# Kernel optimization log

Hardware: AMD Instinct MI355X
Metric: run time of the kernel (lower is better)

Reference implementation:

```python
import jax, jax.numpy as jnp
import numpy as np

NU, NB, NI, D, L = 30000, 10000, 60000, 64, 2
E_UB, E_UI, E_BI = 400000, 800000, 800000


def _graphs(rng, na, nb, ne):
    # random bipartite graph [na, nb] with ne edges; returns Laplacian-normalized
    # symmetric propagation edge list (size 2*ne over na+nb nodes) and the
    # row-normalized aggregation edge values (original MultiCBR preprocessing).
    r = rng.integers(0, na, ne).astype(np.int32)
    c = rng.integers(0, nb, ne).astype(np.int32)
    da = np.bincount(r, minlength=na).astype(np.float32)  # row degrees
    db = np.bincount(c, minlength=nb).astype(np.float32)  # col degrees
    lap = 1.0 / ((np.sqrt(da[r]) + 1e-8) * (np.sqrt(db[c]) + 1e-8))
    prop_rows = np.concatenate([r, c + na]).astype(np.int32)
    prop_cols = np.concatenate([c + na, r]).astype(np.int32)
    prop_vals = np.concatenate([lap, lap]).astype(np.float32)
    agg_vals = (1.0 / (da[r] + 1e-8)).astype(np.float32)  # diag(1/rowsum) @ G
    return prop_rows, prop_cols, prop_vals, r, c, agg_vals


def setup_inputs() -> dict:
    rng = np.random.default_rng(0)
    key = jax.random.key(0)
    ku, kb, ki = jax.random.split(key, 3)
    ub = _graphs(rng, NU, NB, E_UB)
    ui = _graphs(rng, NU, NI, E_UI)
    bi = _graphs(rng, NB, NI, E_BI)
    xav = lambda n: float(np.sqrt(2.0 / (n + D)))  # xavier_normal std
    return {
        "users_feature": jax.random.normal(ku, (NU, D), jnp.float32) * xav(NU),
        "bundles_feature": jax.random.normal(kb, (NB, D), jnp.float32) * xav(NB),
        "items_feature": jax.random.normal(ki, (NI, D), jnp.float32) * xav(NI),
        "ub_rows": jnp.asarray(ub[0]), "ub_cols": jnp.asarray(ub[1]), "ub_vals": jnp.asarray(ub[2]),
        "ui_rows": jnp.asarray(ui[0]), "ui_cols": jnp.asarray(ui[1]), "ui_vals": jnp.asarray(ui[2]),
        "bi_rows": jnp.asarray(bi[0]), "bi_cols": jnp.asarray(bi[1]), "bi_vals": jnp.asarray(bi[2]),
        "bi_agg_rows": jnp.asarray(bi[3]), "bi_agg_cols": jnp.asarray(bi[4]), "bi_agg_vals": jnp.asarray(bi[5]),
        "ui_agg_rows": jnp.asarray(ui[3]), "ui_agg_cols": jnp.asarray(ui[4]), "ui_agg_vals": jnp.asarray(ui[5]),
        "ub_layer_coefs": jnp.full((L + 1,), 1.0 / (L + 1), jnp.float32),
        "ui_layer_coefs": jnp.full((L + 1,), 1.0 / (L + 1), jnp.float32),
        "bi_layer_coefs": jnp.full((L + 1,), 1.0 / (L + 1), jnp.float32),
        "modal_coefs": jnp.asarray([0.4, 0.3, 0.3], jnp.float32),
    }


def _spmm(rows, cols, vals, feat, n):
    # sparse [n, n_src] @ feat : gather + weighted segment-sum
    return jax.ops.segment_sum(vals[:, None] * feat[cols], rows, num_segments=n)


def _l2norm(x):
    # torch F.normalize(p=2, dim=1)
    return x / jnp.maximum(jnp.linalg.norm(x, axis=1, keepdims=True), 1e-12)


def _propagate(rows, cols, vals, a, b, coefs):
    feat = jnp.concatenate([a, b], axis=0)
    n = feat.shape[0]
    acc = coefs[0] * feat  # layer-0 (un-normalized, as in original)
    for i in range(L):
        feat = _spmm(rows, cols, vals, feat, n)
        acc = acc + coefs[i + 1] * _l2norm(feat)
    return acc[: a.shape[0]], acc[a.shape[0]:]


def reference(users_feature, bundles_feature, items_feature,
              ub_rows, ub_cols, ub_vals,
              ui_rows, ui_cols, ui_vals,
              bi_rows, bi_cols, bi_vals,
              bi_agg_rows, bi_agg_cols, bi_agg_vals,
              ui_agg_rows, ui_agg_cols, ui_agg_vals,
              ub_layer_coefs, ui_layer_coefs, bi_layer_coefs, modal_coefs):
    # test=True path of get_multi_modal_representations
    ub_u, ub_b = _propagate(ub_rows, ub_cols, ub_vals, users_feature, bundles_feature, ub_layer_coefs)
    ui_u, ui_i = _propagate(ui_rows, ui_cols, ui_vals, users_feature, items_feature, ui_layer_coefs)
    bi_b, bi_i = _propagate(bi_rows, bi_cols, bi_vals, bundles_feature, items_feature, bi_layer_coefs)
    ui_b = _spmm(bi_agg_rows, bi_agg_cols, bi_agg_vals, ui_i, NB)  # BI_agg @ UI_items
    bi_u = _spmm(ui_agg_rows, ui_agg_cols, ui_agg_vals, bi_i, NU)  # UI_agg @ BI_items
    users_rep = modal_coefs[0] * ub_u + modal_coefs[1] * ui_u + modal_coefs[2] * bi_u
    bundles_rep = modal_coefs[0] * ub_b + modal_coefs[1] * ui_b + modal_coefs[2] * bi_b
    return users_rep, bundles_rep
```

## Files before the change

kernel.cpp:

```cpp
#include <hip/hip_runtime.h>

#define D 64
#define WIN 2048

__device__ __forceinline__ float blo(unsigned u) { return __uint_as_float(u << 16); }
__device__ __forceinline__ float bhi(unsigned u) { return __uint_as_float(u & 0xffff0000u); }
__device__ __forceinline__ unsigned rne(float f) {
    unsigned u = __float_as_uint(f);
    return (u + 0x7fffu + ((u >> 16) & 1u)) >> 16;
}
__device__ __forceinline__ unsigned packbf(float a, float b) {
    unsigned ub = __float_as_uint(b);
    return rne(a) | ((ub + 0x7fffu + ((ub >> 16) & 1u)) & 0xffff0000u);
}
__device__ __forceinline__ void add4(float4* p, float a, float b, float c, float d) {
    float4 o = *p; o.x += a; o.y += b; o.z += c; o.w += d; *p = o;
}

__global__ void to_bf16_kernel(const float* __restrict__ u, const float* __restrict__ b,
                               const float* __restrict__ it,
                               unsigned* __restrict__ SU, unsigned* __restrict__ SB,
                               unsigned* __restrict__ SI, int nU2, int nB2, int nI2) {
    int i = blockIdx.x * 256 + threadIdx.x;
    if (i < nU2) {
        float2 f = ((const float2*)u)[i];
        SU[i] = packbf(f.x, f.y);
    } else if (i < nU2 + nB2) {
        int j = i - nU2;
        float2 f = ((const float2*)b)[j];
        SB[j] = packbf(f.x, f.y);
    } else if (i < nU2 + nB2 + nI2) {
        int j = i - nU2 - nB2;
        float2 f = ((const float2*)it)[j];
        SI[j] = packbf(f.x, f.y);
    }
}

__global__ void hist_kernel(const int* __restrict__ r0, const int* __restrict__ r1,
                            const int* __restrict__ r2,
                            int ne0, int ne1, int ne2, int n0, int n1, int n2,
                            int* __restrict__ histG) {
    __shared__ int h[512];
    int t = threadIdx.x;
    int g = blockIdx.x >> 8, blk = blockIdx.x & 255;
    const int* rows = (g == 0) ? r0 : (g == 1) ? r1 : r2;
    int ne = (g == 0) ? ne0 : (g == 1) ? ne1 : ne2;
    unsigned n = (unsigned)((g == 0) ? n0 : (g == 1) ? n1 : n2);
    h[t] = 0; h[t + 256] = 0;
    __syncthreads();
    int C = (ne + 255) >> 8;
    int e0 = blk * C, e1 = min(ne, e0 + C);
    for (int e = e0 + t; e < e1; e += 256) {
        unsigned b = ((unsigned)rows[e] << 9) / n;
        atomicAdd(&h[b], 1);
    }
    __syncthreads();
    histG[(((g << 9) | t) << 8) | blk] = h[t];
    histG[(((g << 9) | (t + 256)) << 8) | blk] = h[t + 256];
}

__global__ void scan1_kernel(const int* __restrict__ deg, int* __restrict__ rs,
                             int* __restrict__ bsum, int n) {
    __shared__ int tmp[256];
    int t = threadIdx.x;
    int g = blockIdx.x * 256 + t;
    int v = (g < n) ? deg[g] : 0;
    tmp[t] = v;
    __syncthreads();
    for (int off = 1; off < 256; off <<= 1) {
        int x = (t >= off) ? tmp[t - off] : 0;
        __syncthreads();
        tmp[t] += x;
        __syncthreads();
    }
    if (g < n) rs[g] = tmp[t] - v;
    if (t == 255) bsum[blockIdx.x] = tmp[255];
}

__global__ void scan2_kernel(int* __restrict__ bsum, int B) {
    __shared__ int tmp[2048];
    int t = threadIdx.x;
    int v0 = (t < B) ? bsum[t] : 0;
    int v1 = (t + 1024 < B) ? bsum[t + 1024] : 0;
    tmp[t] = v0; tmp[t + 1024] = v1;
    __syncthreads();
    for (int off = 1; off < 2048; off <<= 1) {
        int a0 = (t >= off) ? tmp[t - off] : 0;
        int a1 = ((t + 1024) >= off) ? tmp[t + 1024 - off] : 0;
        __syncthreads();
        tmp[t] += a0; tmp[t + 1024] += a1;
        __syncthreads();
    }
    if (t < B) bsum[t] = tmp[t] - v0;
    if (t + 1024 < B) bsum[t + 1024] = tmp[t + 1024] - v1;
}

__global__ void scan3_kernel(int* __restrict__ rs, const int* __restrict__ bsum, int n) {
    int g = blockIdx.x * blockDim.x + threadIdx.x;
    if (g < n) rs[g] += bsum[g >> 8];
}

__global__ void bucket_scatter_kernel(const int* __restrict__ r0, const int* __restrict__ c0,
                                      const int* __restrict__ r1, const int* __restrict__ c1,
                                      const int* __restrict__ r2, const int* __restrict__ c2,
                                      int ne0, int ne1, int ne2, int n0, int n1, int n2,
                                      const int* __restrict__ hofs, unsigned* __restrict__ ebuf) {
    __shared__ int cur[512];
    int t = threadIdx.x;
    int g = blockIdx.x >> 8, blk = blockIdx.x & 255;
    const int* rows = (g == 0) ? r0 : (g == 1) ? r1 : r2;
    const int* cols = (g == 0) ? c0 : (g == 1) ? c1 : c2;
    int ne = (g == 0) ? ne0 : (g == 1) ? ne1 : ne2;
    int n  = (g == 0) ? n0  : (g == 1) ? n1  : n2;
    cur[t] = hofs[(((g << 9) | t) << 8) | blk];
    cur[t + 256] = hofs[(((g << 9) | (t + 256)) << 8) | blk];
    __syncthreads();
    int C = (ne + 255) >> 8;
    int e0 = blk * C, e1 = min(ne, e0 + C);
    for (int e = e0 + t; e < e1; e += 256) {
        int r = rows[e];
        unsigned b = ((unsigned)r << 9) / (unsigned)n;
        int rb0 = ((int)b * n + 511) >> 9;
        int pos = atomicAdd(&cur[b], 1);
        ebuf[pos] = ((unsigned)(r - rb0) << 23) | (unsigned)cols[e];
    }
}

__global__ void sort_bucket_kernel(const unsigned* __restrict__ ebuf, const int* __restrict__ hofs,
                                   int* __restrict__ rs0, int* __restrict__ rs1, int* __restrict__ rs2,
                                   float* __restrict__ isd0, float* __restrict__ isd1,
                                   float* __restrict__ isd2, int* __restrict__ ccol,
                                   int ne0, int ne1, int ne2, int n0, int n1, int n2) {
    __shared__ int cnt[256];
    __shared__ int pfx[256];
    int t = threadIdx.x;
    int g = blockIdx.x >> 9, b = blockIdx.x & 511;
    int ne = (g == 0) ? ne0 : (g == 1) ? ne1 : ne2;
    int n  = (g == 0) ? n0  : (g == 1) ? n1  : n2;
    int O  = (g == 0) ? 0   : (g == 1) ? ne0 : ne0 + ne1;
    int*   rs  = (g == 0) ? rs0  : (g == 1) ? rs1  : rs2;
    float* isd = (g == 0) ? isd0 : (g == 1) ? isd1 : isd2;
    int rb0 = (b * n + 511) >> 9;
    int rb1 = ((b + 1) * n + 511) >> 9;
    int R = rb1 - rb0;
    cnt[t] = 0;
    __syncthreads();
    int base = hofs[((g << 9) | b) << 8];
    int end  = (b == 511) ? (O + ne) : hofs[((g << 9) | (b + 1)) << 8];
    for (int e = base + t; e < end; e += 256)
        atomicAdd(&cnt[ebuf[e] >> 23], 1);
    __syncthreads();
    pfx[t] = cnt[t];
    __syncthreads();
    for (int off = 1; off < 256; off <<= 1) {
        int v = (t >= off) ? pfx[t - off] : 0;
        __syncthreads();
        pfx[t] += v;
        __syncthreads();
    }
    int c0 = cnt[t], ex = pfx[t] - c0;
    if (t < R) {
        rs[rb0 + t] = base + ex - O;
        isd[rb0 + t] = 1.0f / (sqrtf((float)c0) + 1e-8f);
    }
    __syncthreads();
    cnt[t] = base + ex;
    __syncthreads();
    for (int e = base + t; e < end; e += 256) {
        unsigned p = ebuf[e];
        int pos = atomicAdd(&cnt[p >> 23], 1);
        ccol[pos] = (int)(p & 0x7fffffu);
    }
    if (b == 511 && t == 0) rs[n] = ne;
}

__device__ __forceinline__ int row_deg(int list, int r, const int* rs_ui, const int* rs_bi,
                                       const int* rs_ub, int n_ui, int NU) {
    const int* rs; int rr;
    if (list == 0) { if (r < n_ui) { rs = rs_ui; rr = r; } else { rs = rs_bi; rr = r - n_ui; } }
    else if (list == 1) { rs = rs_ub; rr = r; }
    else { if (r < NU) { rs = rs_ui; rr = r; } else { rs = rs_bi; rr = r - NU; } }
    return rs[rr + 1] - rs[rr];
}

__global__ void winsort_kernel(const int* __restrict__ rs_ui, const int* __restrict__ rs_bi,
                               const int* __restrict__ rs_ub,
                               int n_ui, int NU, int n0, int n1, int n2,
                               int w0, int w1,
                               int* __restrict__ perm0, int* __restrict__ perm1,
                               int* __restrict__ perm2) {
    __shared__ int hist[256];
    __shared__ int pfx[256];
    int t = threadIdx.x;
    int blk = blockIdx.x, list, wbase, n; int* perm;
    if (blk < w0)           { list = 0; wbase = blk * WIN;             n = n0; perm = perm0; }
    else if (blk < w0 + w1) { list = 1; wbase = (blk - w0) * WIN;      n = n1; perm = perm1; }
    else                    { list = 2; wbase = (blk - w0 - w1) * WIN; n = n2; perm = perm2; }
    hist[t] = 0;
    __syncthreads();
    int lim = min(n - wbase, WIN);
    int bins[8], ranks[8];
#pragma unroll
    for (int i = 0; i < 8; ++i) {
        int rr = i * 256 + t;
        if (rr < lim) {
            int d = row_deg(list, wbase + rr, rs_ui, rs_bi, rs_ub, n_ui, NU);
            int b = 255 - min(d, 255);
            bins[i] = b;
            ranks[i] = atomicAdd(&hist[b], 1);
        } else bins[i] = -1;
    }
    __syncthreads();
    int h = hist[t];
    pfx[t] = h;
    __syncthreads();
    for (int off = 1; off < 256; off <<= 1) {
        int x = (t >= off) ? pfx[t - off] : 0;
        __syncthreads();
        pfx[t] += x;
        __syncthreads();
    }
    hist[t] = pfx[t] - h;
    __syncthreads();
#pragma unroll
    for (int i = 0; i < 8; ++i)
        if (bins[i] >= 0) perm[wbase + hist[bins[i]] + ranks[i]] = wbase + i * 256 + t;
}

struct GA {
    const int* rs; const int* ccol; const float* isd;
    const unsigned* srcA; const unsigned* srcB; int na;
    const float* inA; const float* inB;
    unsigned* feat_out; float* dst0; void* dst1;
    const float* coefs; const float* modalp; int mi; int n;
};

template <bool FIRST, bool A0, bool A1, bool BF16D1>
__global__ void spmm_norm_kernel(GA A, GA B, const int* __restrict__ perm, int ntot) {
    int lane = threadIdx.x & 63;
    int row = (blockIdx.x * (blockDim.x >> 6) + (threadIdx.x >> 6)) * 8 + (lane >> 3);
    if (row >= ntot) return;
    row = perm[row];
    GA G; int r;
    if (row < A.n) { G = A; r = row; }
    else           { G = B; r = row - A.n; if (r >= G.n) return; }
    int q = lane & 7;
    int s = G.rs[r], e = G.rs[r + 1];
    float isr = G.isd[r];
    const unsigned* src; int coff;
    if (FIRST && r < G.na) { src = G.srcB; coff = G.na; }
    else                   { src = G.srcA; coff = 0; }
    src += (q << 2);
    const int* cc = G.ccol;
    const float* isdp = G.isd;
    float a[8];
#pragma unroll
    for (int j = 0; j < 8; ++j) a[j] = 0.f;
    int k = s;
    for (; k + 3 < e; k += 4) {
        int c0 = cc[k], c1 = cc[k + 1], c2 = cc[k + 2], c3 = cc[k + 3];
        uint4 f0 = *(const uint4*)(src + (size_t)(c0 - coff) * 32);
        uint4 f1 = *(const uint4*)(src + (size_t)(c1 - coff) * 32);
        uint4 f2 = *(const uint4*)(src + (size_t)(c2 - coff) * 32);
        uint4 f3 = *(const uint4*)(src + (size_t)(c3 - coff) * 32);
        if (FIRST) {
            float v0 = isdp[c0], v1 = isdp[c1], v2 = isdp[c2], v3 = isdp[c3];
            a[0] = fmaf(v0, blo(f0.x), a[0]); a[1] = fmaf(v0, bhi(f0.x), a[1]);
            a[2] = fmaf(v0, blo(f0.y), a[2]); a[3] = fmaf(v0, bhi(f0.y), a[3]);
            a[4] = fmaf(v0, blo(f0.z), a[4]); a[5] = fmaf(v0, bhi(f0.z), a[5]);
            a[6] = fmaf(v0, blo(f0.w), a[6]); a[7] = fmaf(v0, bhi(f0.w), a[7]);
            a[0] = fmaf(v1, blo(f1.x), a[0]); a[1] = fmaf(v1, bhi(f1.x), a[1]);
            a[2] = fmaf(v1, blo(f1.y), a[2]); a[3] = fmaf(v1, bhi(f1.y), a[3]);
            a[4] = fmaf(v1, blo(f1.z), a[4]); a[5] = fmaf(v1, bhi(f1.z), a[5]);
            a[6] = fmaf(v1, blo(f1.w), a[6]); a[7] = fmaf(v1, bhi(f1.w), a[7]);
            a[0] = fmaf(v2, blo(f2.x), a[0]); a[1] = fmaf(v2, bhi(f2.x), a[1]);
            a[2] = fmaf(v2, blo(f2.y), a[2]); a[3] = fmaf(v2, bhi(f2.y), a[3]);
            a[4] = fmaf(v2, blo(f2.z), a[4]); a[5] = fmaf(v2, bhi(f2.z), a[5]);
            a[6] = fmaf(v2, blo(f2.w), a[6]); a[7] = fmaf(v2, bhi(f2.w), a[7]);
            a[0] = fmaf(v3, blo(f3.x), a[0]); a[1] = fmaf(v3, bhi(f3.x), a[1]);
            a[2] = fmaf(v3, blo(f3.y), a[2]); a[3] = fmaf(v3, bhi(f3.y), a[3]);
            a[4] = fmaf(v3, blo(f3.z), a[4]); a[5] = fmaf(v3, bhi(f3.z), a[5]);
            a[6] = fmaf(v3, blo(f3.w), a[6]); a[7] = fmaf(v3, bhi(f3.w), a[7]);
        } else {
            a[0] += blo(f0.x) + blo(f1.x); a[1] += bhi(f0.x) + bhi(f1.x);
            a[2] += blo(f0.y) + blo(f1.y); a[3] += bhi(f0.y) + bhi(f1.y);
            a[4] += blo(f0.z) + blo(f1.z); a[5] += bhi(f0.z) + bhi(f1.z);
            a[6] += blo(f0.w) + blo(f1.w); a[7] += bhi(f0.w) + bhi(f1.w);
            a[0] += blo(f2.x) + blo(f3.x); a[1] += bhi(f2.x) + bhi(f3.x);
            a[2] += blo(f2.y) + blo(f3.y); a[3] += bhi(f2.y) + bhi(f3.y);
            a[4] += blo(f2.z) + blo(f3.z); a[5] += bhi(f2.z) + bhi(f3.z);
            a[6] += blo(f2.w) + blo(f3.w); a[7] += bhi(f2.w) + bhi(f3.w);
        }
    }
    for (; k + 1 < e; k += 2) {
        int c0 = cc[k], c1 = cc[k + 1];
        uint4 f0 = *(const uint4*)(src + (size_t)(c0 - coff) * 32);
        uint4 f1 = *(const uint4*)(src + (size_t)(c1 - coff) * 32);
        if (FIRST) {
            float v0 = isdp[c0], v1 = isdp[c1];
            a[0] = fmaf(v0, blo(f0.x), a[0]); a[1] = fmaf(v0, bhi(f0.x), a[1]);
            a[2] = fmaf(v0, blo(f0.y), a[2]); a[3] = fmaf(v0, bhi(f0.y), a[3]);
            a[4] = fmaf(v0, blo(f0.z), a[4]); a[5] = fmaf(v0, bhi(f0.z), a[5]);
            a[6] = fmaf(v0, blo(f0.w), a[6]); a[7] = fmaf(v0, bhi(f0.w), a[7]);
            a[0] = fmaf(v1, blo(f1.x), a[0]); a[1] = fmaf(v1, bhi(f1.x), a[1]);
            a[2] = fmaf(v1, blo(f1.y), a[2]); a[3] = fmaf(v1, bhi(f1.y), a[3]);
            a[4] = fmaf(v1, blo(f1.z), a[4]); a[5] = fmaf(v1, bhi(f1.z), a[5]);
            a[6] = fmaf(v1, blo(f1.w), a[6]); a[7] = fmaf(v1, bhi(f1.w), a[7]);
        } else {
            a[0] += blo(f0.x) + blo(f1.x); a[1] += bhi(f0.x) + bhi(f1.x);
            a[2] += blo(f0.y) + blo(f1.y); a[3] += bhi(f0.y) + bhi(f1.y);
            a[4] += blo(f0.z) + blo(f1.z); a[5] += bhi(f0.z) + bhi(f1.z);
            a[6] += blo(f0.w) + blo(f1.w); a[7] += bhi(f0.w) + bhi(f1.w);
        }
    }
    if (k < e) {
        int c0 = cc[k];
        uint4 f0 = *(const uint4*)(src + (size_t)(c0 - coff) * 32);
        if (FIRST) {
            float v0 = isdp[c0];
            a[0] = fmaf(v0, blo(f0.x), a[0]); a[1] = fmaf(v0, bhi(f0.x), a[1]);
            a[2] = fmaf(v0, blo(f0.y), a[2]); a[3] = fmaf(v0, bhi(f0.y), a[3]);
            a[4] = fmaf(v0, blo(f0.z), a[4]); a[5] = fmaf(v0, bhi(f0.z), a[5]);
            a[6] = fmaf(v0, blo(f0.w), a[6]); a[7] = fmaf(v0, bhi(f0.w), a[7]);
        } else {
            a[0] += blo(f0.x); a[1] += bhi(f0.x);
            a[2] += blo(f0.y); a[3] += bhi(f0.y);
            a[4] += blo(f0.z); a[5] += bhi(f0.z);
            a[6] += blo(f0.w); a[7] += bhi(f0.w);
        }
    }
    float s2 = 0.f;
#pragma unroll
    for (int j = 0; j < 8; ++j) s2 += a[j] * a[j];
    s2 += __shfl_xor(s2, 1, 64);
    s2 += __shfl_xor(s2, 2, 64);
    s2 += __shfl_xor(s2, 4, 64);
    float inv = 1.0f / fmaxf(sqrtf(s2), 1e-12f);
    float mm = G.modalp[G.mi];
    size_t ro = (size_t)r * D + (q << 3);
    float ctb[8];
    if (FIRST) {
        float isr2 = isr * isr;
        uint4 fw;
        fw.x = packbf(isr2 * a[0], isr2 * a[1]);
        fw.y = packbf(isr2 * a[2], isr2 * a[3]);
        fw.z = packbf(isr2 * a[4], isr2 * a[5]);
        fw.w = packbf(isr2 * a[6], isr2 * a[7]);
        *(uint4*)(G.feat_out + (size_t)r * 32 + (q << 2)) = fw;
        const float* ib = (r < G.na) ? (G.inA + ro) : (G.inB + (size_t)(r - G.na) * D + (q << 3));
        float4 a0 = *(const float4*)ib;
        float4 a1 = *(const float4*)(ib + 4);
        float c0 = G.coefs[0], c1m = G.coefs[1] * inv;
        ctb[0] = mm * fmaf(c0, a0.x, c1m * a[0]);
        ctb[1] = mm * fmaf(c0, a0.y, c1m * a[1]);
        ctb[2] = mm * fmaf(c0, a0.z, c1m * a[2]);
        ctb[3] = mm * fmaf(c0, a0.w, c1m * a[3]);
        ctb[4] = mm * fmaf(c0, a1.x, c1m * a[4]);
        ctb[5] = mm * fmaf(c0, a1.y, c1m * a[5]);
        ctb[6] = mm * fmaf(c0, a1.z, c1m * a[6]);
        ctb[7] = mm * fmaf(c0, a1.w, c1m * a[7]);
    } else {
        float mc = mm * G.coefs[2] * inv;
#pragma unroll
        for (int j = 0; j < 8; ++j) ctb[j] = mc * a[j];
    }
    if (r < G.na) {
        if (A0) {
            *(float4*)(G.dst0 + ro) = make_float4(ctb[0], ctb[1], ctb[2], ctb[3]);
            *(float4*)(G.dst0 + ro + 4) = make_float4(ctb[4], ctb[5], ctb[6], ctb[7]);
        } else {
            add4((float4*)(G.dst0 + ro), ctb[0], ctb[1], ctb[2], ctb[3]);
            add4((float4*)(G.dst0 + ro + 4), ctb[4], ctb[5], ctb[6], ctb[7]);
        }
    } else if (BF16D1) {
        unsigned* p = (unsigned*)G.dst1 + (size_t)(r - G.na) * 32 + (q << 2);
        if (!A1) {
            uint4 cur = *(const uint4*)p;
            ctb[0] += blo(cur.x); ctb[1] += bhi(cur.x);
            ctb[2] += blo(cur.y); ctb[3] += bhi(cur.y);
            ctb[4] += blo(cur.z); ctb[5] += bhi(cur.z);
            ctb[6] += blo(cur.w); ctb[7] += bhi(cur.w);
        }
        uint4 w;
        w.x = packbf(ctb[0], ctb[1]); w.y = packbf(ctb[2], ctb[3]);
        w.z = packbf(ctb[4], ctb[5]); w.w = packbf(ctb[6], ctb[7]);
        *(uint4*)p = w;
    } else {
        float* d1 = (float*)G.dst1 + (size_t)(r - G.na) * D + (q << 3);
        add4((float4*)d1, ctb[0], ctb[1], ctb[2], ctb[3]);
        add4((float4*)(d1 + 4), ctb[4], ctb[5], ctb[6], ctb[7]);
    }
}

__global__ void agg2_kernel(const int* __restrict__ rsA, const int* __restrict__ ccA,
                            const unsigned* __restrict__ sA, float* __restrict__ oA,
                            int naA, int nA,
                            const int* __restrict__ rsB, const int* __restrict__ ccB,
                            const unsigned* __restrict__ sB, float* __restrict__ oB,
                            int naB, int nB, const int* __restrict__ perm) {
    int lane = threadIdx.x & 63;
    int row = (blockIdx.x * (blockDim.x >> 6) + (threadIdx.x >> 6)) * 8 + (lane >> 3);
    if (row >= nA + nB) return;
    row = perm[row];
    const int* rs; const int* cc; const unsigned* src; float* out; int na; int r;
    if (row < nA) { rs = rsA; cc = ccA; src = sA; out = oA; na = naA; r = row; }
    else          { rs = rsB; cc = ccB; src = sB; out = oB; na = naB; r = row - nA; }
    int q = lane & 7;
    src += (q << 2);
    int s = rs[r], e = rs[r + 1];
    float a[8];
#pragma unroll
    for (int j = 0; j < 8; ++j) a[j] = 0.f;
    int k = s;
    for (; k + 3 < e; k += 4) {
        int c0 = cc[k] - na, c1 = cc[k + 1] - na, c2 = cc[k + 2] - na, c3 = cc[k + 3] - na;
        uint4 f0 = *(const uint4*)(src + (size_t)c0 * 32);
        uint4 f1 = *(const uint4*)(src + (size_t)c1 * 32);
        uint4 f2 = *(const uint4*)(src + (size_t)c2 * 32);
        uint4 f3 = *(const uint4*)(src + (size_t)c3 * 32);
        a[0] += blo(f0.x) + blo(f1.x); a[1] += bhi(f0.x) + bhi(f1.x);
        a[2] += blo(f0.y) + blo(f1.y); a[3] += bhi(f0.y) + bhi(f1.y);
        a[4] += blo(f0.z) + blo(f1.z); a[5] += bhi(f0.z) + bhi(f1.z);
        a[6] += blo(f0.w) + blo(f1.w); a[7] += bhi(f0.w) + bhi(f1.w);
        a[0] += blo(f2.x) + blo(f3.x); a[1] += bhi(f2.x) + bhi(f3.x);
        a[2] += blo(f2.y) + blo(f3.y); a[3] += bhi(f2.y) + bhi(f3.y);
        a[4] += blo(f2.z) + blo(f3.z); a[5] += bhi(f2.z) + bhi(f3.z);
        a[6] += blo(f2.w) + blo(f3.w); a[7] += bhi(f2.w) + bhi(f3.w);
    }
    for (; k + 1 < e; k += 2) {
        int c0 = cc[k] - na, c1 = cc[k + 1] - na;
        uint4 f0 = *(const uint4*)(src + (size_t)c0 * 32);
        uint4 f1 = *(const uint4*)(src + (size_t)c1 * 32);
        a[0] += blo(f0.x) + blo(f1.x); a[1] += bhi(f0.x) + bhi(f1.x);
        a[2] += blo(f0.y) + blo(f1.y); a[3] += bhi(f0.y) + bhi(f1.y);
        a[4] += blo(f0.z) + blo(f1.z); a[5] += bhi(f0.z) + bhi(f1.z);
        a[6] += blo(f0.w) + blo(f1.w); a[7] += bhi(f0.w) + bhi(f1.w);
    }
    if (k < e) {
        int c0 = cc[k] - na;
        uint4 f0 = *(const uint4*)(src + (size_t)c0 * 32);
        a[0] += blo(f0.x); a[1] += bhi(f0.x);
        a[2] += blo(f0.y); a[3] += bhi(f0.y);
        a[4] += blo(f0.z); a[5] += bhi(f0.z);
        a[6] += blo(f0.w); a[7] += bhi(f0.w);
    }
    float ad = 1.0f / ((float)(e - s) + 1e-8f);
    float* p = out + (size_t)r * D + (q << 3);
    add4((float4*)p, ad * a[0], ad * a[1], ad * a[2], ad * a[3]);
    add4((float4*)(p + 4), ad * a[4], ad * a[5], ad * a[6], ad * a[7]);
}

extern "C" void kernel_launch(void* const* d_in, const int* in_sizes, int n_in,
                              void* d_out, int out_size, void* d_ws, size_t ws_size,
                              hipStream_t stream) {
    const float* users   = (const float*)d_in[0];
    const float* bundles = (const float*)d_in[1];
    const float* items   = (const float*)d_in[2];
    const int*   ub_rows = (const int*)d_in[3];
    const int*   ub_cols = (const int*)d_in[4];
    const int*   ui_rows = (const int*)d_in[6];
    const int*   ui_cols = (const int*)d_in[7];
    const int*   bi_rows = (const int*)d_in[9];
    const int*   bi_cols = (const int*)d_in[10];
    const float* ub_coefs = (const float*)d_in[18];
    const float* ui_coefs = (const float*)d_in[19];
    const float* bi_coefs = (const float*)d_in[20];
    const float* modal    = (const float*)d_in[21];

    const int NU_ = in_sizes[0] / D;
    const int NB_ = in_sizes[1] / D;
    const int NI_ = in_sizes[2] / D;
    const int ne_ub = in_sizes[3];
    const int ne_ui = in_sizes[6];
    const int ne_bi = in_sizes[9];

    const int n_ui = NU_ + NI_;
    const int n_bi = NB_ + NI_;
    const int n_ub = NU_ + NB_;

    float* out = (float*)d_out;

    int*      rs_ui  = (int*)d_ws;
    int*      rs_bi  = rs_ui + 90112;
    int*      rs_ub  = rs_bi + 70144;
    float*    isd_ui = (float*)(rs_ub + 40192);
    float*    isd_bi = isd_ui + 90112;
    float*    isd_ub = isd_bi + 70144;
    int*      hofs   = (int*)(isd_ub + 40192);
    int*      bsum   = hofs + 393280;
    int*      ccol   = bsum + 2048;
    int*      histG  = ccol;
    unsigned* SU     = (unsigned*)(ccol + 4000000);
    unsigned* SB     = SU + 960000;
    unsigned* SI     = SB + 320000;
    unsigned* ovl    = SI + 1920000;
    unsigned* ebuf   = ovl;
    unsigned* sfB_ui = ovl;
    unsigned* sfB_bi = sfB_ui + 2880000;
    unsigned* IT1b   = sfB_bi + 2240000;
    unsigned* IT2b   = IT1b + 1920000;
    unsigned* sfB_ub = IT1b;

    int* ccol_ui = ccol;
    int* ccol_bi = ccol + ne_ui;
    int* ccol_ub = ccol + ne_ui + ne_bi;

    const int n0 = n_ui + n_bi, n1 = n_ub, n2 = NU_ + NB_;
    int* perm0 = hofs;
    int* perm1 = perm0 + n0;
    int* perm2 = perm1 + n1;

    float* out_u = out;
    float* out_b = out + (size_t)NU_ * D;

    {
        int tot2 = (NU_ + NB_ + NI_) * 32;
        to_bf16_kernel<<<(tot2 + 255) / 256, 256, 0, stream>>>(
            users, bundles, items, SU, SB, SI, NU_ * 32, NB_ * 32, NI_ * 32);
    }

    hist_kernel<<<768, 256, 0, stream>>>(ui_rows, bi_rows, ub_rows,
                                         ne_ui, ne_bi, ne_ub, n_ui, n_bi, n_ub, histG);
    scan1_kernel<<<1536, 256, 0, stream>>>(histG, hofs, bsum, 393216);
    scan2_kernel<<<1, 1024, 0, stream>>>(bsum, 1536);
    scan3_kernel<<<1536, 256, 0, stream>>>(hofs, bsum, 393216);
    bucket_scatter_kernel<<<768, 256, 0, stream>>>(
        ui_rows, ui_cols, bi_rows, bi_cols, ub_rows, ub_cols,
        ne_ui, ne_bi, ne_ub, n_ui, n_bi, n_ub, hofs, ebuf);
    sort_bucket_kernel<<<1536, 256, 0, stream>>>(
        ebuf, hofs, rs_ui, rs_bi, rs_ub, isd_ui, isd_bi, isd_ub, ccol,
        ne_ui, ne_bi, ne_ub, n_ui, n_bi, n_ub);

    {
        int w0 = (n0 + WIN - 1) / WIN, w1 = (n1 + WIN - 1) / WIN, w2 = (n2 + WIN - 1) / WIN;
        winsort_kernel<<<w0 + w1 + w2, 256, 0, stream>>>(
            rs_ui, rs_bi, rs_ub, n_ui, NU_, n0, n1, n2, w0, w1, perm0, perm1, perm2);
    }

    GA gUI = { rs_ui, ccol_ui, isd_ui, SU, SI, NU_, users, items,
               sfB_ui, out_u, (void*)IT1b, ui_coefs, modal, 1, n_ui };
    GA gBI = { rs_bi, ccol_bi, isd_bi, SB, SI, NB_, bundles, items,
               sfB_bi, out_b, (void*)IT2b, bi_coefs, modal, 2, n_bi };
    GA gUB = { rs_ub, ccol_ub, isd_ub, SU, SB, NU_, users, bundles,
               sfB_ub, out_u, (void*)out_b, ub_coefs, modal, 0, n_ub };
    GA gUI2 = gUI; gUI2.srcA = sfB_ui;
    GA gBI2 = gBI; gBI2.srcA = sfB_bi;
    GA gUB2 = gUB; gUB2.srcA = sfB_ub;

    int ntotL = n_ui + n_bi;
    spmm_norm_kernel<true,  true,  true,  true ><<<(ntotL + 31) / 32, 256, 0, stream>>>(gUI,  gBI,  perm0, ntotL);
    spmm_norm_kernel<false, false, false, true ><<<(ntotL + 31) / 32, 256, 0, stream>>>(gUI2, gBI2, perm0, ntotL);

    agg2_kernel<<<(NU_ + NB_ + 31) / 32, 256, 0, stream>>>(
        rs_ui, ccol_ui, IT2b, out_u, NU_, NU_,
        rs_bi, ccol_bi, IT1b, out_b, NB_, NB_, perm2);

    spmm_norm_kernel<true,  false, false, false><<<(n_ub + 31) / 32, 256, 0, stream>>>(gUB,  gUB,  perm1, n_ub);
    spmm_norm_kernel<false, false, false, false><<<(n_ub + 31) / 32, 256, 0, stream>>>(gUB2, gUB2, perm1, n_ub);
}
```

Measured before the change: 485.0 us.

## Stage bucket scatter and per-bucket sort in shared memory for coalesced writes

The bucket scatter kernel now builds a local histogram and prefix scan, places edges into a shared-memory staging buffer grouped by bucket, then copies each bucket's run to global memory contiguously. The per-bucket sort similarly writes sorted columns into shared memory when the bucket fits and then streams them out. Both aim to replace scattered global writes with coalesced ones, at the cost of an extra pass over the rows, more barriers and large shared-memory allocations that reduce occupancy. The 4-way unrolled gather loops in the SpMM kernels are also removed, leaving the 2-way loop, which lowers register pressure but gives less memory-level parallelism per thread.

```diff
diff --git a/kernel.cpp b/kernel.cpp
--- a/kernel.cpp
+++ b/kernel.cpp
@@ -105,24 +105,53 @@
                                       const int* __restrict__ r2, const int* __restrict__ c2,
                                       int ne0, int ne1, int ne2, int n0, int n1, int n2,
                                       const int* __restrict__ hofs, unsigned* __restrict__ ebuf) {
+    __shared__ unsigned se[8192];
+    __shared__ int h[512];
+    __shared__ int lofs[512];
     __shared__ int cur[512];
+    __shared__ int gb[512];
+    __shared__ int tmp[512];
     int t = threadIdx.x;
     int g = blockIdx.x >> 8, blk = blockIdx.x & 255;
     const int* rows = (g == 0) ? r0 : (g == 1) ? r1 : r2;
     const int* cols = (g == 0) ? c0 : (g == 1) ? c1 : c2;
     int ne = (g == 0) ? ne0 : (g == 1) ? ne1 : ne2;
     int n  = (g == 0) ? n0  : (g == 1) ? n1  : n2;
-    cur[t] = hofs[(((g << 9) | t) << 8) | blk];
-    cur[t + 256] = hofs[(((g << 9) | (t + 256)) << 8) | blk];
+    h[t] = 0; h[t + 256] = 0;
     __syncthreads();
     int C = (ne + 255) >> 8;
     int e0 = blk * C, e1 = min(ne, e0 + C);
     for (int e = e0 + t; e < e1; e += 256) {
+        unsigned b = ((unsigned)rows[e] << 9) / (unsigned)n;
+        atomicAdd(&h[b], 1);
+    }
+    __syncthreads();
+    tmp[t] = h[t]; tmp[t + 256] = h[t + 256];
+    __syncthreads();
+    for (int off = 1; off < 512; off <<= 1) {
+        int a0 = (t >= off) ? tmp[t - off] : 0;
+        int a1 = ((t + 256) >= off) ? tmp[t + 256 - off] : 0;
+        __syncthreads();
+        tmp[t] += a0; tmp[t + 256] += a1;
+        __syncthreads();
+    }
+    lofs[t] = tmp[t] - h[t]; lofs[t + 256] = tmp[t + 256] - h[t + 256];
+    cur[t] = lofs[t]; cur[t + 256] = lofs[t + 256];
+    gb[t] = hofs[(((g << 9) | t) << 8) | blk];
+    gb[t + 256] = hofs[(((g << 9) | (t + 256)) << 8) | blk];
+    __syncthreads();
+    for (int e = e0 + t; e < e1; e += 256) {
         int r = rows[e];
         unsigned b = ((unsigned)r << 9) / (unsigned)n;
-        int rb0 = ((int)b * n + 511) >> 9;
-        int pos = atomicAdd(&cur[b], 1);
-        ebuf[pos] = ((unsigned)(r - rb0) << 23) | (unsigned)cols[e];
+        int rb0v = ((int)b * n + 511) >> 9;
+        int p = atomicAdd(&cur[b], 1);
+        se[p] = ((unsigned)(r - rb0v) << 23) | (unsigned)cols[e];
+    }
+    __syncthreads();
+    int wid = t >> 6, lane = t & 63;
+    for (int b = wid; b < 512; b += 4) {
+        int lb = lofs[b], len = cur[b] - lb, gbb = gb[b];
+        for (int j = lane; j < len; j += 64) ebuf[gbb + j] = se[lb + j];
     }
 }
 
@@ -133,6 +162,7 @@
                                    int ne0, int ne1, int ne2, int n0, int n1, int n2) {
     __shared__ int cnt[256];
     __shared__ int pfx[256];
+    __shared__ int scol[8192];
     int t = threadIdx.x;
     int g = blockIdx.x >> 9, b = blockIdx.x & 511;
     int ne = (g == 0) ? ne0 : (g == 1) ? ne1 : ne2;
@@ -147,6 +177,7 @@
     __syncthreads();
     int base = hofs[((g << 9) | b) << 8];
     int end  = (b == 511) ? (O + ne) : hofs[((g << 9) | (b + 1)) << 8];
+    int E = end - base;
     for (int e = base + t; e < end; e += 256)
         atomicAdd(&cnt[ebuf[e] >> 23], 1);
     __syncthreads();
@@ -164,12 +195,18 @@
         isd[rb0 + t] = 1.0f / (sqrtf((float)c0) + 1e-8f);
     }
     __syncthreads();
-    cnt[t] = base + ex;
+    bool fits = (E <= 8192);
+    cnt[t] = fits ? ex : (base + ex);
     __syncthreads();
     for (int e = base + t; e < end; e += 256) {
         unsigned p = ebuf[e];
         int pos = atomicAdd(&cnt[p >> 23], 1);
-        ccol[pos] = (int)(p & 0x7fffffu);
+        if (fits) scol[pos] = (int)(p & 0x7fffffu);
+        else      ccol[pos] = (int)(p & 0x7fffffu);
+    }
+    if (fits) {
+        __syncthreads();
+        for (int j = t; j < E; j += 256) ccol[base + j] = scol[j];
     }
     if (b == 511 && t == 0) rs[n] = ne;
 }
@@ -257,41 +294,6 @@
 #pragma unroll
     for (int j = 0; j < 8; ++j) a[j] = 0.f;
     int k = s;
-    for (; k + 3 < e; k += 4) {
-        int c0 = cc[k], c1 = cc[k + 1], c2 = cc[k + 2], c3 = cc[k + 3];
-        uint4 f0 = *(const uint4*)(src + (size_t)(c0 - coff) * 32);
-        uint4 f1 = *(const uint4*)(src + (size_t)(c1 - coff) * 32);
-        uint4 f2 = *(const uint4*)(src + (size_t)(c2 - coff) * 32);
-        uint4 f3 = *(const uint4*)(src + (size_t)(c3 - coff) * 32);
-        if (FIRST) {
-            float v0 = isdp[c0], v1 = isdp[c1], v2 = isdp[c2], v3 = isdp[c3];
-            a[0] = fmaf(v0, blo(f0.x), a[0]); a[1] = fmaf(v0, bhi(f0.x), a[1]);
-            a[2] = fmaf(v0, blo(f0.y), a[2]); a[3] = fmaf(v0, bhi(f0.y), a[3]);
-            a[4] = fmaf(v0, blo(f0.z), a[4]); a[5] = fmaf(v0, bhi(f0.z), a[5]);
-            a[6] = fmaf(v0, blo(f0.w), a[6]); a[7] = fmaf(v0, bhi(f0.w), a[7]);
-            a[0] = fmaf(v1, blo(f1.x), a[0]); a[1] = fmaf(v1, bhi(f1.x), a[1]);
-            a[2] = fmaf(v1, blo(f1.y), a[2]); a[3] = fmaf(v1, bhi(f1.y), a[3]);
-            a[4] = fmaf(v1, blo(f1.z), a[4]); a[5] = fmaf(v1, bhi(f1.z), a[5]);
-            a[6] = fmaf(v1, blo(f1.w), a[6]); a[7] = fmaf(v1, bhi(f1.w), a[7]);
-            a[0] = fmaf(v2, blo(f2.x), a[0]); a[1] = fmaf(v2, bhi(f2.x), a[1]);
-            a[2] = fmaf(v2, blo(f2.y), a[2]); a[3] = fmaf(v2, bhi(f2.y), a[3]);
-            a[4] = fmaf(v2, blo(f2.z), a[4]); a[5] = fmaf(v2, bhi(f2.z), a[5]);
-            a[6] = fmaf(v2, blo(f2.w), a[6]); a[7] = fmaf(v2, bhi(f2.w), a[7]);
-            a[0] = fmaf(v3, blo(f3.x), a[0]); a[1] = fmaf(v3, bhi(f3.x), a[1]);
-            a[2] = fmaf(v3, blo(f3.y), a[2]); a[3] = fmaf(v3, bhi(f3.y), a[3]);
-            a[4] = fmaf(v3, blo(f3.z), a[4]); a[5] = fmaf(v3, bhi(f3.z), a[5]);
-            a[6] = fmaf(v3, blo(f3.w), a[6]); a[7] = fmaf(v3, bhi(f3.w), a[7]);
-        } else {
-            a[0] += blo(f0.x) + blo(f1.x); a[1] += bhi(f0.x) + bhi(f1.x);
-            a[2] += blo(f0.y) + blo(f1.y); a[3] += bhi(f0.y) + bhi(f1.y);
-            a[4] += blo(f0.z) + blo(f1.z); a[5] += bhi(f0.z) + bhi(f1.z);
-            a[6] += blo(f0.w) + blo(f1.w); a[7] += bhi(f0.w) + bhi(f1.w);
-            a[0] += blo(f2.x) + blo(f3.x); a[1] += bhi(f2.x) + bhi(f3.x);
-            a[2] += blo(f2.y) + blo(f3.y); a[3] += bhi(f2.y) + bhi(f3.y);
-            a[4] += blo(f2.z) + blo(f3.z); a[5] += bhi(f2.z) + bhi(f3.z);
-            a[6] += blo(f2.w) + blo(f3.w); a[7] += bhi(f2.w) + bhi(f3.w);
-        }
-    }
     for (; k + 1 < e; k += 2) {
         int c0 = cc[k], c1 = cc[k + 1];
         uint4 f0 = *(const uint4*)(src + (size_t)(c0 - coff) * 32);
@@ -412,21 +414,6 @@
 #pragma unroll
     for (int j = 0; j < 8; ++j) a[j] = 0.f;
     int k = s;
-    for (; k + 3 < e; k += 4) {
-        int c0 = cc[k] - na, c1 = cc[k + 1] - na, c2 = cc[k + 2] - na, c3 = cc[k + 3] - na;
-        uint4 f0 = *(const uint4*)(src + (size_t)c0 * 32);
-        uint4 f1 = *(const uint4*)(src + (size_t)c1 * 32);
-        uint4 f2 = *(const uint4*)(src + (size_t)c2 * 32);
-        uint4 f3 = *(const uint4*)(src + (size_t)c3 * 32);
-        a[0] += blo(f0.x) + blo(f1.x); a[1] += bhi(f0.x) + bhi(f1.x);
-        a[2] += blo(f0.y) + blo(f1.y); a[3] += bhi(f0.y) + bhi(f1.y);
-        a[4] += blo(f0.z) + blo(f1.z); a[5] += bhi(f0.z) + bhi(f1.z);
-        a[6] += blo(f0.w) + blo(f1.w); a[7] += bhi(f0.w) + bhi(f1.w);
-        a[0] += blo(f2.x) + blo(f3.x); a[1] += bhi(f2.x) + bhi(f3.x);
-        a[2] += blo(f2.y) + blo(f3.y); a[3] += bhi(f2.y) + bhi(f3.y);
-        a[4] += blo(f2.z) + blo(f3.z); a[5] += bhi(f2.z) + bhi(f3.z);
-        a[6] += blo(f2.w) + blo(f3.w); a[7] += bhi(f2.w) + bhi(f3.w);
-    }
     for (; k + 1 < e; k += 2) {
         int c0 = cc[k] - na, c1 = cc[k + 1] - na;
         uint4 f0 = *(const uint4*)(src + (size_t)c0 * 32);
```

New measurement: 526.4 us. +8.5%, slower.
